# Kernel tuning notes

Hardware: AMD Instinct MI355X
Metric: run time of the kernel (lower is better)

The kernel has to match this reference:

```python
import jax, jax.numpy as jnp
import numpy as np

B, S, HID = 1, 2048, 4096
H, HKV = 32, 8
D = HID // H          # 128
G = H // HKV          # 4 query heads per kv head (GQA)


def setup_inputs() -> dict:
    key = jax.random.key(0)
    ks = jax.random.split(key, 5)
    hidden_states = jax.random.normal(ks[0], (B, S, HID), dtype=jnp.float32)
    # additive causal mask: 0 on/below diagonal, large negative above
    causal = jnp.tril(jnp.ones((S, S), dtype=bool))
    attention_mask = jnp.where(causal, 0.0, -1e9).astype(jnp.float32)[None, None]
    sc = 0.02
    wq = jax.random.normal(ks[1], (HID, H * D), dtype=jnp.float32) * sc
    wk = jax.random.normal(ks[2], (HID, HKV * D), dtype=jnp.float32) * sc
    wv = jax.random.normal(ks[3], (HID, HKV * D), dtype=jnp.float32) * sc
    wo = jax.random.normal(ks[4], (H * D, HID), dtype=jnp.float32) * sc
    return {"hidden_states": hidden_states, "attention_mask": attention_mask,
            "wq": wq, "wk": wk, "wv": wv, "wo": wo}


def reference(hidden_states, attention_mask, wq, wk, wv, wo):
    # projections (lora_rank=0 path: plain dense, no bias)
    q = hidden_states @ wq                      # [B,S,H*D]
    k = hidden_states @ wk                      # [B,S,HKV*D]
    v = hidden_states @ wv                      # [B,S,HKV*D]
    # split heads; group query heads by their kv head: head h -> (h//G, h%G)
    q = q.reshape(B, S, HKV, G, D).transpose(0, 2, 3, 1, 4)   # [B,HKV,G,S,D]
    k = k.reshape(B, S, HKV, D).transpose(0, 2, 1, 3)          # [B,HKV,S,D]
    v = v.reshape(B, S, HKV, D).transpose(0, 2, 1, 3)          # [B,HKV,S,D]
    scale = 1.0 / jnp.sqrt(jnp.float32(D))
    # explicit S x S scores (as in source), with GQA kv broadcast over G
    scores = jnp.einsum('bkgsd,bktd->bkgst', q, k) * scale     # [B,HKV,G,S,S]
    scores = scores + attention_mask[:, :, None]               # broadcast over G
    probs = jax.nn.softmax(scores, axis=-1)
    attn = jnp.einsum('bkgst,bktd->bkgsd', probs, v)           # [B,HKV,G,S,D]
    attn = attn.transpose(0, 3, 1, 2, 4).reshape(B, S, H * D)  # [B,S,H*D]
    return attn @ wo                                           # [B,S,HID]
```

## Files before the change

kernel.cpp:

```cpp
#include <hip/hip_runtime.h>
#include <hip/hip_bf16.h>

#define S_LEN 2048
#define HID 4096
#define NH 32
#define NKV 8
#define HD 128
#define LDQKV 6144

typedef __bf16 bf16x8 __attribute__((ext_vector_type(8)));
typedef __bf16 bf16x4 __attribute__((ext_vector_type(4)));
typedef float f32x4 __attribute__((ext_vector_type(4)));

#define GLD16(gp, lp)                                                                   \
    __builtin_amdgcn_global_load_lds((const __attribute__((address_space(1))) void*)(gp), \
                                     (__attribute__((address_space(3))) void*)(lp), 16, 0, 0)

__global__ void cast_bf16_kernel(const float* __restrict__ x, __bf16* __restrict__ y, int n) {
    int i = (blockIdx.x * blockDim.x + threadIdx.x) * 4;
    if (i < n) {
        float4 v = *reinterpret_cast<const float4*>(x + i);
        bf16x4 o;
        o.x = (__bf16)v.x; o.y = (__bf16)v.y; o.z = (__bf16)v.z; o.w = (__bf16)v.w;
        *reinterpret_cast<bf16x4*>(y + i) = o;
    }
}

__global__ void transpose_cast_kernel(const float* __restrict__ W, __bf16* __restrict__ WT,
                                      int K, int N, float scale) {
    __shared__ float tile[32][33];
    int bx = blockIdx.x;
    int by = blockIdx.y;
    int tx = threadIdx.x;
    int ty = threadIdx.y;
    int n = bx * 32 + tx;
#pragma unroll
    for (int i = 0; i < 4; i++) {
        int k = by * 32 + ty + i * 8;
        tile[ty + i * 8][tx] = W[(size_t)k * N + n];
    }
    __syncthreads();
    int k2 = by * 32 + tx;
#pragma unroll
    for (int i = 0; i < 4; i++) {
        int n2 = bx * 32 + ty + i * 8;
        WT[(size_t)n2 * K + k2] = (__bf16)(tile[tx][ty + i * 8] * scale);
    }
}

__global__ void transpose_bf16_kernel(const __bf16* __restrict__ V, int ldin,
                                      __bf16* __restrict__ VT, int ldout) {
    __shared__ __bf16 tile[32][33];
    int bx = blockIdx.x;
    int by = blockIdx.y;
    int tx = threadIdx.x;
    int ty = threadIdx.y;
#pragma unroll
    for (int i = 0; i < 4; i++)
        tile[ty + i * 8][tx] = V[(size_t)(by * 32 + ty + i * 8) * ldin + bx * 32 + tx];
    __syncthreads();
#pragma unroll
    for (int i = 0; i < 4; i++)
        VT[(size_t)(bx * 32 + ty + i * 8) * ldout + by * 32 + tx] = tile[tx][ty + i * 8];
}

template <typename OUT_T>
__global__ __launch_bounds__(256) void gemm_bt_kernel(const __bf16* __restrict__ A, int lda,
                                                      const __bf16* __restrict__ BT, int ldb,
                                                      OUT_T* __restrict__ C, int ldc, int K) {
    __shared__ __bf16 As[128 * 32];
    __shared__ __bf16 Bs[128 * 32];
    int n0 = blockIdx.x * 128;
    int m0 = blockIdx.y * 128;
    int tid = threadIdx.x;
    int wave = tid >> 6, lane = tid & 63, quad = lane >> 4, l16 = lane & 15;
    int wm = (wave >> 1) * 64, wn = (wave & 1) * 64;
    int j0 = wave * 128 + lane;

    f32x4 acc[4][4] = {};

    for (int kb = 0; kb < K; kb += 32) {
        __syncthreads();
#pragma unroll
        for (int q = 0; q < 2; q++) {
            int j = j0 + q * 64;
            int row = j >> 2, col8 = (j & 3) * 8;
            GLD16(&A[(size_t)(m0 + row) * lda + kb + col8], &As[j * 8]);
            GLD16(&BT[(size_t)(n0 + row) * ldb + kb + col8], &Bs[j * 8]);
        }
        __syncthreads();
        bf16x8 af[4], bfr[4];
#pragma unroll
        for (int mt = 0; mt < 4; mt++)
            af[mt] = *reinterpret_cast<const bf16x8*>(&As[(wm + mt * 16 + l16) * 32 + quad * 8]);
#pragma unroll
        for (int nt = 0; nt < 4; nt++)
            bfr[nt] = *reinterpret_cast<const bf16x8*>(&Bs[(wn + nt * 16 + l16) * 32 + quad * 8]);
#pragma unroll
        for (int mt = 0; mt < 4; mt++)
#pragma unroll
            for (int nt = 0; nt < 4; nt++)
                acc[mt][nt] = __builtin_amdgcn_mfma_f32_16x16x32_bf16(af[mt], bfr[nt],
                                                                      acc[mt][nt], 0, 0, 0);
    }

#pragma unroll
    for (int mt = 0; mt < 4; mt++)
#pragma unroll
        for (int nt = 0; nt < 4; nt++)
#pragma unroll
            for (int r = 0; r < 4; r++) {
                int row = m0 + wm + mt * 16 + quad * 4 + r;
                int col = n0 + wn + nt * 16 + l16;
                C[(size_t)row * ldc + col] = (OUT_T)acc[mt][nt][r];
            }
}

__global__ __launch_bounds__(256) void attn_kernel(const __bf16* __restrict__ QKV,
                                                   const __bf16* __restrict__ VT,
                                                   __bf16* __restrict__ Ao,
                                                   __bf16* __restrict__ Opart,
                                                   float* __restrict__ Lp) {
    __shared__ __bf16 Ks[64 * 128];
    __shared__ __bf16 Vs[128 * 64];
    __shared__ __bf16 Pl[4][2][16 * 72];
    int x = blockIdx.x;
    int qt, c;
    if (x < 32) { qt = 31 - (x >> 1); c = x & 1; }
    else        { qt = 47 - x;        c = 0;     }
    int hp = blockIdx.y;
    int kvh = hp >> 1;
    int h0 = kvh * 4 + (hp & 1) * 2;
    int t0 = c ? 16 : 0;
    int t1 = c ? qt : min(qt, 15);
    int tid = threadIdx.x;
    int wave = tid >> 6, lane = tid & 63, quad = lane >> 4, l16 = lane & 15;
    int wq = qt * 64 + wave * 16;
    const __bf16* Kb = QKV + HID + (size_t)kvh * HD;
    const __bf16* Vt = VT + (size_t)kvh * HD * S_LEN;

    bf16x8 qf[2][4];
#pragma unroll
    for (int h = 0; h < 2; h++)
#pragma unroll
        for (int ks = 0; ks < 4; ks++)
            qf[h][ks] = *reinterpret_cast<const bf16x8*>(
                &QKV[(size_t)(wq + l16) * LDQKV + (h0 + h) * HD + ks * 32 + quad * 8]);

    bf16x8 ones;
#pragma unroll
    for (int j = 0; j < 8; j++) ones[j] = (__bf16)1.0f;

    f32x4 acc_o[2][8] = {};
    f32x4 lacc[2] = {};

    for (int t = t0; t <= t1; t++) {
        int kv0 = t << 6;
        bool diag = (t == qt);
        __syncthreads();
#pragma unroll
        for (int i = 0; i < 4; i++) {
            int cc = i * 256 + tid;
            int row = cc >> 4, sub = cc & 15;
            int col8 = sub ^ (row & 15);
            GLD16(&Kb[(size_t)(kv0 + row) * LDQKV + col8 * 8], &Ks[cc * 8]);
        }
#pragma unroll
        for (int i = 0; i < 4; i++) {
            int cc = i * 256 + tid;
            int row = cc >> 3, sub = cc & 7;
            int col8 = sub ^ (row & 7);
            GLD16(&Vt[(size_t)row * S_LEN + kv0 + col8 * 8], &Vs[cc * 8]);
        }
        __syncthreads();

        f32x4 sacc[2][4] = {};
#pragma unroll
        for (int ks = 0; ks < 4; ks++) {
            bf16x8 kf[4];
#pragma unroll
            for (int n = 0; n < 4; n++) {
                int row = n * 16 + l16;
                int sub = (ks * 4 + quad) ^ l16;
                kf[n] = *reinterpret_cast<const bf16x8*>(&Ks[row * 128 + sub * 8]);
            }
#pragma unroll
            for (int n = 0; n < 4; n++) {
                sacc[0][n] = __builtin_amdgcn_mfma_f32_16x16x32_bf16(qf[0][ks], kf[n],
                                                                     sacc[0][n], 0, 0, 0);
                sacc[1][n] = __builtin_amdgcn_mfma_f32_16x16x32_bf16(qf[1][ks], kf[n],
                                                                     sacc[1][n], 0, 0, 0);
            }
        }
#pragma unroll
        for (int h = 0; h < 2; h++) {
            __bf16* Pw = Pl[wave][h];
#pragma unroll
            for (int r = 0; r < 4; r++) {
                int row = wq + quad * 4 + r;
#pragma unroll
                for (int n = 0; n < 4; n++) {
                    float v = sacc[h][n][r];
                    if (diag) {
                        int col = kv0 + n * 16 + l16;
                        if (col > row) v = -1e30f;
                    }
                    Pw[(quad * 4 + r) * 72 + n * 16 + l16] =
                        (__bf16)__builtin_amdgcn_exp2f(v);
                }
            }
        }
#pragma unroll
        for (int ks = 0; ks < 2; ks++) {
            bf16x8 pf0 = *reinterpret_cast<const bf16x8*>(
                &Pl[wave][0][l16 * 72 + ks * 32 + quad * 8]);
            bf16x8 pf1 = *reinterpret_cast<const bf16x8*>(
                &Pl[wave][1][l16 * 72 + ks * 32 + quad * 8]);
            lacc[0] = __builtin_amdgcn_mfma_f32_16x16x32_bf16(pf0, ones, lacc[0], 0, 0, 0);
            lacc[1] = __builtin_amdgcn_mfma_f32_16x16x32_bf16(pf1, ones, lacc[1], 0, 0, 0);
#pragma unroll
            for (int dn = 0; dn < 8; dn++) {
                int row = dn * 16 + l16;
                int sub = (ks * 4 + quad) ^ (row & 7);
                bf16x8 vf = *reinterpret_cast<const bf16x8*>(&Vs[row * 64 + sub * 8]);
                acc_o[0][dn] = __builtin_amdgcn_mfma_f32_16x16x32_bf16(pf0, vf,
                                                                       acc_o[0][dn], 0, 0, 0);
                acc_o[1][dn] = __builtin_amdgcn_mfma_f32_16x16x32_bf16(pf1, vf,
                                                                       acc_o[1][dn], 0, 0, 0);
            }
        }
    }

    if (qt < 16) {
#pragma unroll
        for (int h = 0; h < 2; h++) {
            float rl[4];
#pragma unroll
            for (int r = 0; r < 4; r++) rl[r] = 1.0f / lacc[h][r];
#pragma unroll
            for (int dn = 0; dn < 8; dn++)
#pragma unroll
                for (int r = 0; r < 4; r++) {
                    int row = wq + quad * 4 + r;
                    int col = (h0 + h) * HD + dn * 16 + l16;
                    Ao[(size_t)row * HID + col] = (__bf16)(acc_o[h][dn][r] * rl[r]);
                }
        }
    } else {
        int s = (qt - 16) * 2 + c;
#pragma unroll
        for (int h = 0; h < 2; h++) {
            size_t base = ((size_t)(h0 + h) * 32 + s) * 64 + wave * 16;
#pragma unroll
            for (int dn = 0; dn < 8; dn++)
#pragma unroll
                for (int r = 0; r < 4; r++)
                    Opart[(base + quad * 4 + r) * 128 + dn * 16 + l16] =
                        (__bf16)acc_o[h][dn][r];
            if (l16 == 0) {
#pragma unroll
                for (int r = 0; r < 4; r++)
                    Lp[base + quad * 4 + r] = lacc[h][r];
            }
        }
    }
}

__global__ __launch_bounds__(256) void attn_combine(const __bf16* __restrict__ Opart,
                                                    const float* __restrict__ Lp,
                                                    __bf16* __restrict__ Ao) {
    int qt = 16 + (int)blockIdx.x;
    int h = blockIdx.y;
    int tid = threadIdx.x;
    size_t b0 = ((size_t)h * 32 + (qt - 16) * 2) * 64;
    size_t b1 = b0 + 64;
#pragma unroll 4
    for (int i = 0; i < 32; i++) {
        int el = i * 256 + tid;
        int rl = el >> 7, col = el & 127;
        float l = Lp[b0 + rl] + Lp[b1 + rl];
        float O = (float)Opart[(b0 + rl) * 128 + col] + (float)Opart[(b1 + rl) * 128 + col];
        int row = qt * 64 + rl;
        Ao[(size_t)row * HID + h * HD + col] = (__bf16)(O / l);
    }
}

extern "C" void kernel_launch(void* const* d_in, const int* in_sizes, int n_in,
                              void* d_out, int out_size, void* d_ws, size_t ws_size,
                              hipStream_t stream) {
    const float* hs = (const float*)d_in[0];
    const float* wq = (const float*)d_in[2];
    const float* wk = (const float*)d_in[3];
    const float* wv = (const float*)d_in[4];
    const float* wo = (const float*)d_in[5];
    float* out = (float*)d_out;

    char* ws = (char*)d_ws;
    __bf16* WqkvT = (__bf16*)(ws + (size_t)0);
    __bf16* Opart = (__bf16*)(ws + (size_t)0);
    float*  Lp    = (float*)(ws + ((size_t)20 << 20));
    __bf16* Xb    = (__bf16*)(ws + ((size_t)48 << 20));
    __bf16* QKV   = (__bf16*)(ws + ((size_t)64 << 20));
    __bf16* VTg   = (__bf16*)(ws + ((size_t)88 << 20));
    __bf16* Ab    = Xb;

    const int nX = S_LEN * HID;
    const float SC2 = 0.12751743f;

    cast_bf16_kernel<<<nX / 4 / 256, 256, 0, stream>>>(hs, Xb, nX);
    transpose_cast_kernel<<<dim3(128, 128), dim3(32, 8), 0, stream>>>(wq, WqkvT, HID, HID, SC2);
    transpose_cast_kernel<<<dim3(32, 128), dim3(32, 8), 0, stream>>>(
        wk, WqkvT + (size_t)4096 * HID, HID, NKV * HD, 1.0f);
    transpose_cast_kernel<<<dim3(32, 128), dim3(32, 8), 0, stream>>>(
        wv, WqkvT + (size_t)5120 * HID, HID, NKV * HD, 1.0f);
    gemm_bt_kernel<__bf16><<<dim3(LDQKV / 128, S_LEN / 128), 256, 0, stream>>>(
        Xb, HID, WqkvT, HID, QKV, LDQKV, HID);
    transpose_bf16_kernel<<<dim3(32, 64), dim3(32, 8), 0, stream>>>(
        QKV + 5120, LDQKV, VTg, S_LEN);
    attn_kernel<<<dim3(48, 16), 256, 0, stream>>>(QKV, VTg, Ab, Opart, Lp);
    attn_combine<<<dim3(16, 32), 256, 0, stream>>>(Opart, Lp, Ab);
    transpose_cast_kernel<<<dim3(128, 128), dim3(32, 8), 0, stream>>>(wo, WqkvT, HID, HID, 1.0f);
    gemm_bt_kernel<float><<<dim3(HID / 128, S_LEN / 128), 256, 0, stream>>>(
        Ab, HID, WqkvT, HID, out, HID, HID);
}
```

Baseline: 550.7 us.

## Widen GEMM K tile, merge QKV weight transposes, vectorize P stores with permuted V

The three Q/K/V weight transpose-casts become one launch using 64x64 tiles with float4 loads and bf16x4 stores, and the Wo transpose uses the same wider kernel. The GEMM K step doubles from 32 to 64, halving the number of barrier pairs per output tile at the cost of twice the shared memory. In attention, probabilities are packed into bf16x4 stores instead of scalar stores. To keep the P·V product correct under that new column order, the V transpose permutes its sequence index to match.

```diff
diff --git a/kernel.cpp b/kernel.cpp
--- a/kernel.cpp
+++ b/kernel.cpp
@@ -26,30 +26,64 @@
     }
 }
 
-__global__ void transpose_cast_kernel(const float* __restrict__ W, __bf16* __restrict__ WT,
-                                      int K, int N, float scale) {
-    __shared__ float tile[32][33];
+__global__ __launch_bounds__(256) void transpose_cast64(const float* __restrict__ W,
+                                                        __bf16* __restrict__ WT,
+                                                        int K, int N, float sc) {
+    __shared__ float tile[64][65];
+    int n0 = blockIdx.x * 64, k0 = blockIdx.y * 64;
+    int tx = threadIdx.x & 15, ty = threadIdx.x >> 4;
+#pragma unroll
+    for (int i = 0; i < 4; i++) {
+        float4 v = *reinterpret_cast<const float4*>(&W[(size_t)(k0 + ty + i * 16) * N + n0 + tx * 4]);
+        tile[ty + i * 16][tx * 4 + 0] = v.x;
+        tile[ty + i * 16][tx * 4 + 1] = v.y;
+        tile[ty + i * 16][tx * 4 + 2] = v.z;
+        tile[ty + i * 16][tx * 4 + 3] = v.w;
+    }
+    __syncthreads();
+#pragma unroll
+    for (int i = 0; i < 4; i++) {
+        int n = ty + i * 16;
+        bf16x4 o;
+#pragma unroll
+        for (int jj = 0; jj < 4; jj++) o[jj] = (__bf16)(tile[tx * 4 + jj][n] * sc);
+        *reinterpret_cast<bf16x4*>(&WT[(size_t)(n0 + n) * K + k0 + tx * 4]) = o;
+    }
+}
+
+__global__ __launch_bounds__(256) void transpose_qkv_kernel(const float* __restrict__ Wq,
+                                                            const float* __restrict__ Wk,
+                                                            const float* __restrict__ Wv,
+                                                            __bf16* __restrict__ WT, float scq) {
+    __shared__ float tile[64][65];
     int bx = blockIdx.x;
-    int by = blockIdx.y;
-    int tx = threadIdx.x;
-    int ty = threadIdx.y;
-    int n = bx * 32 + tx;
+    const float* W; int N; int nbase; size_t obase; float sc;
+    if (bx < 64)      { W = Wq; N = 4096; nbase = bx * 64;        obase = 0;                  sc = scq; }
+    else if (bx < 80) { W = Wk; N = 1024; nbase = (bx - 64) * 64; obase = (size_t)4096 * HID; sc = 1.f; }
+    else              { W = Wv; N = 1024; nbase = (bx - 80) * 64; obase = (size_t)5120 * HID; sc = 1.f; }
+    int k0 = blockIdx.y * 64;
+    int tx = threadIdx.x & 15, ty = threadIdx.x >> 4;
 #pragma unroll
     for (int i = 0; i < 4; i++) {
-        int k = by * 32 + ty + i * 8;
-        tile[ty + i * 8][tx] = W[(size_t)k * N + n];
+        float4 v = *reinterpret_cast<const float4*>(&W[(size_t)(k0 + ty + i * 16) * N + nbase + tx * 4]);
+        tile[ty + i * 16][tx * 4 + 0] = v.x;
+        tile[ty + i * 16][tx * 4 + 1] = v.y;
+        tile[ty + i * 16][tx * 4 + 2] = v.z;
+        tile[ty + i * 16][tx * 4 + 3] = v.w;
     }
     __syncthreads();
-    int k2 = by * 32 + tx;
 #pragma unroll
     for (int i = 0; i < 4; i++) {
-        int n2 = bx * 32 + ty + i * 8;
-        WT[(size_t)n2 * K + k2] = (__bf16)(tile[tx][ty + i * 8] * scale);
-    }
-}
-
-__global__ void transpose_bf16_kernel(const __bf16* __restrict__ V, int ldin,
-                                      __bf16* __restrict__ VT, int ldout) {
+        int n = ty + i * 16;
+        bf16x4 o;
+#pragma unroll
+        for (int jj = 0; jj < 4; jj++) o[jj] = (__bf16)(tile[tx * 4 + jj][n] * sc);
+        *reinterpret_cast<bf16x4*>(&WT[obase + (size_t)(nbase + n) * HID + k0 + tx * 4]) = o;
+    }
+}
+
+__global__ void transpose_vperm_kernel(const __bf16* __restrict__ V, int ldin,
+                                       __bf16* __restrict__ VT, int ldout) {
     __shared__ __bf16 tile[32][33];
     int bx = blockIdx.x;
     int by = blockIdx.y;
@@ -59,49 +93,55 @@
     for (int i = 0; i < 4; i++)
         tile[ty + i * 8][tx] = V[(size_t)(by * 32 + ty + i * 8) * ldin + bx * 32 + tx];
     __syncthreads();
+    int s = by * 32 + tx;
+    int sp = (s & ~63) | ((s & 15) << 2) | ((s >> 4) & 3);
 #pragma unroll
     for (int i = 0; i < 4; i++)
-        VT[(size_t)(bx * 32 + ty + i * 8) * ldout + by * 32 + tx] = tile[tx][ty + i * 8];
+        VT[(size_t)(bx * 32 + ty + i * 8) * ldout + sp] = tile[tx][ty + i * 8];
 }
 
 template <typename OUT_T>
 __global__ __launch_bounds__(256) void gemm_bt_kernel(const __bf16* __restrict__ A, int lda,
                                                       const __bf16* __restrict__ BT, int ldb,
                                                       OUT_T* __restrict__ C, int ldc, int K) {
-    __shared__ __bf16 As[128 * 32];
-    __shared__ __bf16 Bs[128 * 32];
+    __shared__ __bf16 As[128 * 64];
+    __shared__ __bf16 Bs[128 * 64];
     int n0 = blockIdx.x * 128;
     int m0 = blockIdx.y * 128;
     int tid = threadIdx.x;
     int wave = tid >> 6, lane = tid & 63, quad = lane >> 4, l16 = lane & 15;
     int wm = (wave >> 1) * 64, wn = (wave & 1) * 64;
-    int j0 = wave * 128 + lane;
 
     f32x4 acc[4][4] = {};
 
-    for (int kb = 0; kb < K; kb += 32) {
+    for (int kb = 0; kb < K; kb += 64) {
         __syncthreads();
 #pragma unroll
-        for (int q = 0; q < 2; q++) {
-            int j = j0 + q * 64;
-            int row = j >> 2, col8 = (j & 3) * 8;
+        for (int q = 0; q < 4; q++) {
+            int j = tid + q * 256;
+            int row = j >> 3, col8 = (j & 7) * 8;
             GLD16(&A[(size_t)(m0 + row) * lda + kb + col8], &As[j * 8]);
             GLD16(&BT[(size_t)(n0 + row) * ldb + kb + col8], &Bs[j * 8]);
         }
         __syncthreads();
-        bf16x8 af[4], bfr[4];
-#pragma unroll
-        for (int mt = 0; mt < 4; mt++)
-            af[mt] = *reinterpret_cast<const bf16x8*>(&As[(wm + mt * 16 + l16) * 32 + quad * 8]);
-#pragma unroll
-        for (int nt = 0; nt < 4; nt++)
-            bfr[nt] = *reinterpret_cast<const bf16x8*>(&Bs[(wn + nt * 16 + l16) * 32 + quad * 8]);
-#pragma unroll
-        for (int mt = 0; mt < 4; mt++)
+#pragma unroll
+        for (int ks = 0; ks < 2; ks++) {
+            bf16x8 af[4], bfr[4];
+#pragma unroll
+            for (int mt = 0; mt < 4; mt++)
+                af[mt] = *reinterpret_cast<const bf16x8*>(
+                    &As[(wm + mt * 16 + l16) * 64 + ks * 32 + quad * 8]);
 #pragma unroll
             for (int nt = 0; nt < 4; nt++)
-                acc[mt][nt] = __builtin_amdgcn_mfma_f32_16x16x32_bf16(af[mt], bfr[nt],
-                                                                      acc[mt][nt], 0, 0, 0);
+                bfr[nt] = *reinterpret_cast<const bf16x8*>(
+                    &Bs[(wn + nt * 16 + l16) * 64 + ks * 32 + quad * 8]);
+#pragma unroll
+            for (int mt = 0; mt < 4; mt++)
+#pragma unroll
+                for (int nt = 0; nt < 4; nt++)
+                    acc[mt][nt] = __builtin_amdgcn_mfma_f32_16x16x32_bf16(af[mt], bfr[nt],
+                                                                          acc[mt][nt], 0, 0, 0);
+        }
     }
 
 #pragma unroll
@@ -198,6 +238,7 @@
 #pragma unroll
             for (int r = 0; r < 4; r++) {
                 int row = wq + quad * 4 + r;
+                bf16x4 pk;
 #pragma unroll
                 for (int n = 0; n < 4; n++) {
                     float v = sacc[h][n][r];
@@ -205,9 +246,9 @@
                         int col = kv0 + n * 16 + l16;
                         if (col > row) v = -1e30f;
                     }
-                    Pw[(quad * 4 + r) * 72 + n * 16 + l16] =
-                        (__bf16)__builtin_amdgcn_exp2f(v);
+                    pk[n] = (__bf16)__builtin_amdgcn_exp2f(v);
                 }
+                *reinterpret_cast<bf16x4*>(&Pw[(quad * 4 + r) * 72 + l16 * 4]) = pk;
             }
         }
 #pragma unroll
@@ -308,18 +349,14 @@
     const float SC2 = 0.12751743f;
 
     cast_bf16_kernel<<<nX / 4 / 256, 256, 0, stream>>>(hs, Xb, nX);
-    transpose_cast_kernel<<<dim3(128, 128), dim3(32, 8), 0, stream>>>(wq, WqkvT, HID, HID, SC2);
-    transpose_cast_kernel<<<dim3(32, 128), dim3(32, 8), 0, stream>>>(
-        wk, WqkvT + (size_t)4096 * HID, HID, NKV * HD, 1.0f);
-    transpose_cast_kernel<<<dim3(32, 128), dim3(32, 8), 0, stream>>>(
-        wv, WqkvT + (size_t)5120 * HID, HID, NKV * HD, 1.0f);
+    transpose_qkv_kernel<<<dim3(96, 64), 256, 0, stream>>>(wq, wk, wv, WqkvT, SC2);
     gemm_bt_kernel<__bf16><<<dim3(LDQKV / 128, S_LEN / 128), 256, 0, stream>>>(
         Xb, HID, WqkvT, HID, QKV, LDQKV, HID);
-    transpose_bf16_kernel<<<dim3(32, 64), dim3(32, 8), 0, stream>>>(
+    transpose_vperm_kernel<<<dim3(32, 64), dim3(32, 8), 0, stream>>>(
         QKV + 5120, LDQKV, VTg, S_LEN);
     attn_kernel<<<dim3(48, 16), 256, 0, stream>>>(QKV, VTg, Ab, Opart, Lp);
     attn_combine<<<dim3(16, 32), 256, 0, stream>>>(Opart, Lp, Ab);
-    transpose_cast_kernel<<<dim3(128, 128), dim3(32, 8), 0, stream>>>(wo, WqkvT, HID, HID, 1.0f);
+    transpose_cast64<<<dim3(64, 64), 256, 0, stream>>>(wo, WqkvT, HID, HID, 1.0f);
     gemm_bt_kernel<float><<<dim3(HID / 128, S_LEN / 128), 256, 0, stream>>>(
         Ab, HID, WqkvT, HID, out, HID, HID);
 }
```

New measurement: 574.4 us. 1.04x slower.
